# Kernel tuning notes

Measured on AMD Instinct MI355X. Metric: run time of the kernel, lower is better.

Reference implementation:

```python
import jax, jax.numpy as jnp
import numpy as np

EPS = 1e-12  # matches torch euclidean_dist clamp(min=1e-12)


def _euclidean_dist(a, b):
    # pairwise sqrt distances: [N, M]
    d2 = (jnp.sum(a * a, axis=1)[:, None]
          + jnp.sum(b * b, axis=1)[None, :]
          - 2.0 * (a @ b.T))
    return jnp.sqrt(jnp.clip(d2, EPS))


def setup_inputs() -> dict:
    key = jax.random.key(0)
    k1, k2, k3 = jax.random.split(key, 3)
    B, I, E, C = 131072, 512, 128, 64
    x = jax.random.normal(k1, (B, I), dtype=jnp.float32)
    y = jax.random.randint(k2, (B,), 0, C)  # class labels
    W = jax.random.normal(k3, (E, I), dtype=jnp.float32) * 0.02
    b = jnp.zeros((E,), dtype=jnp.float32)
    centroid = jnp.zeros((C, E), dtype=jnp.float32)
    return {"x": x, "y": y, "W": W, "b": b, "centroid": centroid}


def reference(x, y, W, b, centroid):
    # linear projection: [B, E]
    out = x @ W.T + b
    C = centroid.shape[0]
    # fused per-class masked mean (segment mean). flag[i]==0 always in the
    # original module, so the executed update is centroid[i] += mean_i.
    sums = jax.ops.segment_sum(out, y, num_segments=C)            # [C, E]
    counts = jax.ops.segment_sum(jnp.ones(y.shape, out.dtype), y,
                                 num_segments=C)                   # [C]
    means = sums / counts[:, None]
    new_centroid = centroid + means
    # only the final loop iteration's proto_dist / dist survive
    proto_dist = jnp.exp(-0.5 * _euclidean_dist(new_centroid, new_centroid))
    dist = _euclidean_dist(out, new_centroid)                      # [B, C]
    return jax.nn.sigmoid(jnp.exp(-0.5 * dist)), proto_dist
```

## Files before the change

kernel.cpp:

```cpp
#include <hip/hip_runtime.h>
#include <math.h>


typedef __bf16 bf16;
typedef bf16  bf16x4 __attribute__((ext_vector_type(4)));
typedef bf16  bf16x8 __attribute__((ext_vector_type(8)));
typedef float f32x4  __attribute__((ext_vector_type(4)));

#define B_ROWS 131072
#define K_DIM  512
#define E_DIM  128
#define C_CLS  64

#define BM 128
#define BK 64

#define SEG_BLOCKS 256
#define ROWS_PER_SEG (B_ROWS / SEG_BLOCKS)

#define DIST_BLOCKS (B_ROWS / 128)
#define PROTO_BLOCKS 16

__global__ __launch_bounds__(256, 2)
void gemm_kernel(const float* __restrict__ x, const float* __restrict__ W,
                 const float* __restrict__ bias, bf16* __restrict__ outb,
                 float* __restrict__ rnorm)
{
    __shared__ bf16 As[BM * BK];
    __shared__ bf16 Bs[BM * BK];
    __shared__ float lr[BM];

    const int t    = threadIdx.x;
    const int lane = t & 63;
    const int w    = t >> 6;
    const int wr   = w >> 1;
    const int wc   = w & 1;
    const int fr   = lane & 15;
    const int fq   = lane >> 4;
    const long blockRow = (long)blockIdx.x * BM;

    const int srow = t >> 4;
    const int scol = (t & 15) * 4;

    f32x4 acc[4][4] = {};
    if (t < BM) lr[t] = 0.f;

    const float* xg = x + blockRow * K_DIM;

    for (int kt = 0; kt < K_DIM; kt += BK) {
        __syncthreads();
        #pragma unroll
        for (int r = 0; r < 8; ++r) {
            int row = r * 16 + srow;
            f32x4 va = *(const f32x4*)(xg + (long)row * K_DIM + kt + scol);
            f32x4 vb = *(const f32x4*)(W  + (long)row * K_DIM + kt + scol);
            bf16x4 pa = { (bf16)va.x, (bf16)va.y, (bf16)va.z, (bf16)va.w };
            bf16x4 pb = { (bf16)vb.x, (bf16)vb.y, (bf16)vb.z, (bf16)vb.w };
            int byte = row * (BK * 2) + ((scol * 2) ^ ((row & 7) << 4));
            *(bf16x4*)((char*)As + byte) = pa;
            *(bf16x4*)((char*)Bs + byte) = pb;
        }
        __syncthreads();
        #pragma unroll
        for (int kk = 0; kk < 2; ++kk) {
            bf16x8 af[4], bg[4];
            #pragma unroll
            for (int m = 0; m < 4; ++m) {
                int row  = wr * 64 + m * 16 + fr;
                int byte = row * (BK * 2) + (((kk * 32 + fq * 8) * 2) ^ ((row & 7) << 4));
                af[m] = *(const bf16x8*)((const char*)As + byte);
            }
            #pragma unroll
            for (int n = 0; n < 4; ++n) {
                int row  = wc * 64 + n * 16 + fr;
                int byte = row * (BK * 2) + (((kk * 32 + fq * 8) * 2) ^ ((row & 7) << 4));
                bg[n] = *(const bf16x8*)((const char*)Bs + byte);
            }
            #pragma unroll
            for (int m = 0; m < 4; ++m)
                #pragma unroll
                for (int n = 0; n < 4; ++n)
                    acc[m][n] = __builtin_amdgcn_mfma_f32_16x16x32_bf16(
                        af[m], bg[n], acc[m][n], 0, 0, 0);
        }
    }

    float bvv[4];
    #pragma unroll
    for (int n = 0; n < 4; ++n) bvv[n] = bias[wc * 64 + n * 16 + fr];

    #pragma unroll
    for (int m = 0; m < 4; ++m) {
        #pragma unroll
        for (int j = 0; j < 4; ++j) {
            long grow = blockRow + wr * 64 + m * 16 + fq * 4 + j;
            float s = 0.f;
            #pragma unroll
            for (int n = 0; n < 4; ++n) {
                float v = acc[m][n][j] + bvv[n];
                outb[grow * E_DIM + wc * 64 + n * 16 + fr] = (bf16)v;
                s += v * v;
            }
            s += __shfl_xor(s, 1); s += __shfl_xor(s, 2);
            s += __shfl_xor(s, 4); s += __shfl_xor(s, 8);
            if (fr == 0) atomicAdd(&lr[wr * 64 + m * 16 + fq * 4 + j], s);
        }
    }
    __syncthreads();
    if (t < BM) rnorm[blockRow + t] = lr[t];
}

__global__ __launch_bounds__(256)
void segsum_kernel(const bf16* __restrict__ outb, const int* __restrict__ y,
                   float* __restrict__ pw, float* __restrict__ pc)
{
    __shared__ float lsum[C_CLS * E_DIM];
    __shared__ float lcnt[C_CLS];
    const int t = threadIdx.x;
    for (int i = t; i < C_CLS * E_DIM; i += 256) lsum[i] = 0.f;
    if (t < C_CLS) lcnt[t] = 0.f;
    __syncthreads();
    const long base = (long)blockIdx.x * ROWS_PER_SEG;
    const int rsub = t >> 4;
    const int c8   = (t & 15) * 8;
    for (int i = 0; i < ROWS_PER_SEG; i += 16) {
        long row = base + i + rsub;
        int  cls = y[row];
        bf16x8 v = *(const bf16x8*)(outb + row * E_DIM + c8);
        if ((t & 15) == 0) atomicAdd(&lcnt[cls], 1.0f);
        #pragma unroll
        for (int k = 0; k < 8; ++k)
            atomicAdd(&lsum[cls * E_DIM + c8 + k], (float)v[k]);
    }
    __syncthreads();
    for (int i = t; i < C_CLS * E_DIM; i += 256)
        pw[(long)blockIdx.x * (C_CLS * E_DIM) + i] = lsum[i];
    if (t < C_CLS) pc[blockIdx.x * C_CLS + t] = lcnt[t];
}

__global__ __launch_bounds__(256)
void reduce_kernel(const float* __restrict__ pw, float* __restrict__ sums)
{
    int idx = blockIdx.x * 256 + threadIdx.x;
    float s = 0.f;
    for (int j = 0; j < SEG_BLOCKS; ++j) s += pw[(long)j * (C_CLS * E_DIM) + idx];
    sums[idx] = s;
}

__global__ __launch_bounds__(256)
void centroid_kernel(const float* __restrict__ sums, const float* __restrict__ pc,
                     const float* __restrict__ centroid0,
                     float* __restrict__ cent, float* __restrict__ cnorm)
{
    __shared__ float cnt[C_CLS];
    __shared__ float sc[C_CLS * E_DIM];
    const int t = threadIdx.x;
    if (t < C_CLS) {
        float s = 0.f;
        for (int j = 0; j < SEG_BLOCKS; ++j) s += pc[j * C_CLS + t];
        cnt[t] = s;
    }
    __syncthreads();
    for (int i = t; i < C_CLS * E_DIM; i += 256) {
        float v = centroid0[i] + sums[i] / cnt[i >> 7];
        sc[i]   = v;
        cent[i] = v;
    }
    __syncthreads();
    if (t < C_CLS) {
        float s = 0.f;
        for (int e = 0; e < E_DIM; ++e) { float v = sc[t * E_DIM + e]; s += v * v; }
        cnorm[t] = s;
    }
}

__global__ __launch_bounds__(256, 4)
void dist_kernel(const bf16* __restrict__ outb, const float* __restrict__ cent,
                 const float* __restrict__ cnorm, const float* __restrict__ rnorm,
                 float* __restrict__ out0, float* __restrict__ proto)
{
    __shared__ float smemf[C_CLS * 129 + C_CLS + 128];
    const int t = threadIdx.x;

    if (blockIdx.x >= DIST_BLOCKS) {
        float* scf   = smemf;
        float* pnorm = smemf + C_CLS * 129;
        for (int idx = t; idx < C_CLS * E_DIM; idx += 256)
            scf[(idx >> 7) * 129 + (idx & 127)] = cent[idx];
        if (t < C_CLS) pnorm[t] = cnorm[t];
        __syncthreads();
        int p = (blockIdx.x - DIST_BLOCKS) * 256 + t;
        int i = p >> 6, j = p & 63;
        float d = 0.f;
        #pragma unroll 4
        for (int e = 0; e < E_DIM; ++e)
            d += scf[i * 129 + e] * scf[j * 129 + e];
        float d2 = pnorm[i] + pnorm[j] - 2.f * d;
        proto[p] = __expf(-0.5f * sqrtf(fmaxf(d2, 1e-12f)));
        return;
    }

    bf16*  Cs    = (bf16*)smemf;
    float* snorm = smemf + C_CLS * 129;
    float* srnorm = snorm + C_CLS;
    {
        int srw = t >> 5;
        int scl = (t & 31) * 4;
        #pragma unroll
        for (int r = 0; r < 8; ++r) {
            int row = r * 8 + srw;
            f32x4 v = *(const f32x4*)(cent + row * E_DIM + scl);
            bf16x4 pv = { (bf16)v.x, (bf16)v.y, (bf16)v.z, (bf16)v.w };
            int byte = row * (E_DIM * 2) + ((scl * 2) ^ ((row & 7) << 4));
            *(bf16x4*)((char*)Cs + byte) = pv;
        }
        if (t < C_CLS) snorm[t] = cnorm[t];
        if (t < 32) ((f32x4*)srnorm)[t] =
            ((const f32x4*)(rnorm + (long)blockIdx.x * 128))[t];
    }
    const int lane = t & 63;
    const int w    = t >> 6;
    const int fr   = lane & 15;
    const int fq   = lane >> 4;
    const long blkrow = (long)blockIdx.x * 128;
    f32x4 acc[2][4] = {};
    __syncthreads();
    #pragma unroll
    for (int kt = 0; kt < 4; ++kt) {
        bf16x8 af[2];
        #pragma unroll
        for (int m = 0; m < 2; ++m) {
            long row = blkrow + w * 32 + m * 16 + fr;
            af[m] = *(const bf16x8*)(outb + row * E_DIM + kt * 32 + fq * 8);
        }
        #pragma unroll
        for (int n = 0; n < 4; ++n) {
            int row  = n * 16 + fr;
            int byte = row * (E_DIM * 2) + (((kt * 32 + fq * 8) * 2) ^ ((row & 7) << 4));
            bf16x8 bq = *(const bf16x8*)((const char*)Cs + byte);
            acc[0][n] = __builtin_amdgcn_mfma_f32_16x16x32_bf16(af[0], bq, acc[0][n], 0, 0, 0);
            acc[1][n] = __builtin_amdgcn_mfma_f32_16x16x32_bf16(af[1], bq, acc[1][n], 0, 0, 0);
        }
    }
    #pragma unroll
    for (int m = 0; m < 2; ++m) {
        #pragma unroll
        for (int n = 0; n < 4; ++n) {
            int gcol = n * 16 + fr;
            float cn = snorm[gcol];
            #pragma unroll
            for (int j = 0; j < 4; ++j) {
                int lrow = w * 32 + m * 16 + fq * 4 + j;
                float d2 = srnorm[lrow] + cn - 2.f * acc[m][n][j];
                float dist = sqrtf(fmaxf(d2, 1e-12f));
                float ez = __expf(-0.5f * dist);
                out0[(blkrow + lrow) * C_CLS + gcol] = 1.f / (1.f + __expf(-ez));
            }
        }
    }
}

extern "C" void kernel_launch(void* const* d_in, const int* in_sizes, int n_in,
                              void* d_out, int out_size, void* d_ws, size_t ws_size,
                              hipStream_t stream)
{
    const float* x         = (const float*)d_in[0];
    const int*   y         = (const int*)d_in[1];
    const float* W         = (const float*)d_in[2];
    const float* bias      = (const float*)d_in[3];
    const float* centroid0 = (const float*)d_in[4];

    bf16*  outb  = (bf16*)d_ws;
    float* rnorm = (float*)((char*)d_ws + (size_t)B_ROWS * E_DIM * 2);
    float* pw    = rnorm + B_ROWS;
    float* pc    = pw + (long)SEG_BLOCKS * C_CLS * E_DIM;
    float* sums  = pc + SEG_BLOCKS * C_CLS;
    float* cent  = sums + C_CLS * E_DIM;
    float* cnorm = cent + C_CLS * E_DIM;

    float* out0  = (float*)d_out;
    float* proto = out0 + (long)B_ROWS * C_CLS;

    gemm_kernel    <<<B_ROWS / BM, 256, 0, stream>>>(x, W, bias, outb, rnorm);
    segsum_kernel  <<<SEG_BLOCKS, 256, 0, stream>>>(outb, y, pw, pc);
    reduce_kernel  <<<(C_CLS * E_DIM) / 256, 256, 0, stream>>>(pw, sums);
    centroid_kernel<<<1, 256, 0, stream>>>(sums, pc, centroid0, cent, cnorm);
    dist_kernel    <<<DIST_BLOCKS + PROTO_BLOCKS, 256, 0, stream>>>(
        outb, cent, cnorm, rnorm, out0, proto);
}
```

Measured before the change: 192.9 us.

## Double-buffer GEMM tiles, restructure segsum, parallelize reduce and centroid kernels

New measurement: 194.7 us. Within noise of the previous version (+0.9%).

```diff
diff --git a/kernel.cpp b/kernel.cpp
--- a/kernel.cpp
+++ b/kernel.cpp
@@ -3,6 +3,7 @@
 
 
 typedef __bf16 bf16;
+typedef bf16  bf16x2 __attribute__((ext_vector_type(2)));
 typedef bf16  bf16x4 __attribute__((ext_vector_type(4)));
 typedef bf16  bf16x8 __attribute__((ext_vector_type(8)));
 typedef float f32x4  __attribute__((ext_vector_type(4)));
@@ -15,7 +16,7 @@
 #define BM 128
 #define BK 64
 
-#define SEG_BLOCKS 256
+#define SEG_BLOCKS 512
 #define ROWS_PER_SEG (B_ROWS / SEG_BLOCKS)
 
 #define DIST_BLOCKS (B_ROWS / 128)
@@ -26,8 +27,8 @@
                  const float* __restrict__ bias, bf16* __restrict__ outb,
                  float* __restrict__ rnorm)
 {
-    __shared__ bf16 As[BM * BK];
-    __shared__ bf16 Bs[BM * BK];
+    __shared__ bf16 As[2][BM * BK];
+    __shared__ bf16 Bs[2][BM * BK];
     __shared__ float lr[BM];
 
     const int t    = threadIdx.x;
@@ -43,24 +44,41 @@
     const int scol = (t & 15) * 4;
 
     f32x4 acc[4][4] = {};
+    f32x4 va[8], vb[8];
+
+    const float* xg = x + blockRow * K_DIM;
     if (t < BM) lr[t] = 0.f;
 
-    const float* xg = x + blockRow * K_DIM;
-
-    for (int kt = 0; kt < K_DIM; kt += BK) {
-        __syncthreads();
-        #pragma unroll
-        for (int r = 0; r < 8; ++r) {
-            int row = r * 16 + srow;
-            f32x4 va = *(const f32x4*)(xg + (long)row * K_DIM + kt + scol);
-            f32x4 vb = *(const f32x4*)(W  + (long)row * K_DIM + kt + scol);
-            bf16x4 pa = { (bf16)va.x, (bf16)va.y, (bf16)va.z, (bf16)va.w };
-            bf16x4 pb = { (bf16)vb.x, (bf16)vb.y, (bf16)vb.z, (bf16)vb.w };
-            int byte = row * (BK * 2) + ((scol * 2) ^ ((row & 7) << 4));
-            *(bf16x4*)((char*)As + byte) = pa;
-            *(bf16x4*)((char*)Bs + byte) = pb;
-        }
-        __syncthreads();
+    #pragma unroll
+    for (int r = 0; r < 8; ++r) {
+        int row = r * 16 + srow;
+        va[r] = *(const f32x4*)(xg + (long)row * K_DIM + scol);
+        vb[r] = *(const f32x4*)(W  + (long)row * K_DIM + scol);
+    }
+    #pragma unroll
+    for (int r = 0; r < 8; ++r) {
+        int row = r * 16 + srow;
+        bf16x4 pa = { (bf16)va[r].x, (bf16)va[r].y, (bf16)va[r].z, (bf16)va[r].w };
+        bf16x4 pb = { (bf16)vb[r].x, (bf16)vb[r].y, (bf16)vb[r].z, (bf16)vb[r].w };
+        int byte = row * (BK * 2) + ((scol * 2) ^ ((row & 7) << 4));
+        *(bf16x4*)((char*)As[0] + byte) = pa;
+        *(bf16x4*)((char*)Bs[0] + byte) = pb;
+    }
+    __syncthreads();
+
+    for (int kti = 0; kti < K_DIM / BK; ++kti) {
+        const int p = kti & 1;
+        if (kti < K_DIM / BK - 1) {
+            const int kt = (kti + 1) * BK;
+            #pragma unroll
+            for (int r = 0; r < 8; ++r) {
+                int row = r * 16 + srow;
+                va[r] = *(const f32x4*)(xg + (long)row * K_DIM + kt + scol);
+                vb[r] = *(const f32x4*)(W  + (long)row * K_DIM + kt + scol);
+            }
+        }
+        const bf16* Ap = As[p];
+        const bf16* Bp = Bs[p];
         #pragma unroll
         for (int kk = 0; kk < 2; ++kk) {
             bf16x8 af[4], bg[4];
@@ -68,13 +86,13 @@
             for (int m = 0; m < 4; ++m) {
                 int row  = wr * 64 + m * 16 + fr;
                 int byte = row * (BK * 2) + (((kk * 32 + fq * 8) * 2) ^ ((row & 7) << 4));
-                af[m] = *(const bf16x8*)((const char*)As + byte);
+                af[m] = *(const bf16x8*)((const char*)Ap + byte);
             }
             #pragma unroll
             for (int n = 0; n < 4; ++n) {
                 int row  = wc * 64 + n * 16 + fr;
                 int byte = row * (BK * 2) + (((kk * 32 + fq * 8) * 2) ^ ((row & 7) << 4));
-                bg[n] = *(const bf16x8*)((const char*)Bs + byte);
+                bg[n] = *(const bf16x8*)((const char*)Bp + byte);
             }
             #pragma unroll
             for (int m = 0; m < 4; ++m)
@@ -83,6 +101,18 @@
                     acc[m][n] = __builtin_amdgcn_mfma_f32_16x16x32_bf16(
                         af[m], bg[n], acc[m][n], 0, 0, 0);
         }
+        if (kti < K_DIM / BK - 1) {
+            #pragma unroll
+            for (int r = 0; r < 8; ++r) {
+                int row = r * 16 + srow;
+                bf16x4 pa = { (bf16)va[r].x, (bf16)va[r].y, (bf16)va[r].z, (bf16)va[r].w };
+                bf16x4 pb = { (bf16)vb[r].x, (bf16)vb[r].y, (bf16)vb[r].z, (bf16)vb[r].w };
+                int byte = row * (BK * 2) + ((scol * 2) ^ ((row & 7) << 4));
+                *(bf16x4*)((char*)As[p ^ 1] + byte) = pa;
+                *(bf16x4*)((char*)Bs[p ^ 1] + byte) = pb;
+            }
+            __syncthreads();
+        }
     }
 
     float bvv[4];
@@ -116,21 +146,21 @@
 {
     __shared__ float lsum[C_CLS * E_DIM];
     __shared__ float lcnt[C_CLS];
+    __shared__ int   ly[ROWS_PER_SEG];
     const int t = threadIdx.x;
     for (int i = t; i < C_CLS * E_DIM; i += 256) lsum[i] = 0.f;
     if (t < C_CLS) lcnt[t] = 0.f;
-    __syncthreads();
     const long base = (long)blockIdx.x * ROWS_PER_SEG;
-    const int rsub = t >> 4;
-    const int c8   = (t & 15) * 8;
-    for (int i = 0; i < ROWS_PER_SEG; i += 16) {
-        long row = base + i + rsub;
-        int  cls = y[row];
-        bf16x8 v = *(const bf16x8*)(outb + row * E_DIM + c8);
-        if ((t & 15) == 0) atomicAdd(&lcnt[cls], 1.0f);
-        #pragma unroll
-        for (int k = 0; k < 8; ++k)
-            atomicAdd(&lsum[cls * E_DIM + c8 + k], (float)v[k]);
+    if (t < ROWS_PER_SEG) ly[t] = y[base + t];
+    __syncthreads();
+    const int w = t >> 6, lane = t & 63;
+    #pragma unroll 4
+    for (int i = w; i < ROWS_PER_SEG; i += 4) {
+        int cls = ly[i];
+        bf16x2 v = *(const bf16x2*)(outb + (base + i) * E_DIM + lane * 2);
+        atomicAdd(&lsum[cls * E_DIM + lane * 2 + 0], (float)v[0]);
+        atomicAdd(&lsum[cls * E_DIM + lane * 2 + 1], (float)v[1]);
+        if (lane == 0) atomicAdd(&lcnt[cls], 1.f);
     }
     __syncthreads();
     for (int i = t; i < C_CLS * E_DIM; i += 256)
@@ -141,10 +171,22 @@
 __global__ __launch_bounds__(256)
 void reduce_kernel(const float* __restrict__ pw, float* __restrict__ sums)
 {
-    int idx = blockIdx.x * 256 + threadIdx.x;
+    __shared__ float red[256];
+    const int t = threadIdx.x;
+    const int idx = blockIdx.x * 32 + (t & 31);
+    const int js  = t >> 5;
     float s = 0.f;
-    for (int j = 0; j < SEG_BLOCKS; ++j) s += pw[(long)j * (C_CLS * E_DIM) + idx];
-    sums[idx] = s;
+    #pragma unroll 8
+    for (int j = js * 64; j < js * 64 + 64; ++j)
+        s += pw[(long)j * (C_CLS * E_DIM) + idx];
+    red[t] = s;
+    __syncthreads();
+    if (t < 32) {
+        float r = red[t];
+        #pragma unroll
+        for (int k = 1; k < 8; ++k) r += red[t + 32 * k];
+        sums[blockIdx.x * 32 + t] = r;
+    }
 }
 
 __global__ __launch_bounds__(256)
@@ -152,26 +194,32 @@
                      const float* __restrict__ centroid0,
                      float* __restrict__ cent, float* __restrict__ cnorm)
 {
-    __shared__ float cnt[C_CLS];
-    __shared__ float sc[C_CLS * E_DIM];
+    __shared__ float red[256];
+    const int c = blockIdx.x;
     const int t = threadIdx.x;
-    if (t < C_CLS) {
-        float s = 0.f;
-        for (int j = 0; j < SEG_BLOCKS; ++j) s += pc[j * C_CLS + t];
-        cnt[t] = s;
-    }
-    __syncthreads();
-    for (int i = t; i < C_CLS * E_DIM; i += 256) {
-        float v = centroid0[i] + sums[i] / cnt[i >> 7];
-        sc[i]   = v;
-        cent[i] = v;
-    }
-    __syncthreads();
-    if (t < C_CLS) {
-        float s = 0.f;
-        for (int e = 0; e < E_DIM; ++e) { float v = sc[t * E_DIM + e]; s += v * v; }
-        cnorm[t] = s;
-    }
+    float s = pc[t * C_CLS + c] + pc[(t + 256) * C_CLS + c];
+    red[t] = s;
+    __syncthreads();
+    #pragma unroll
+    for (int st = 128; st > 0; st >>= 1) {
+        if (t < st) red[t] += red[t + st];
+        __syncthreads();
+    }
+    const float cnt = red[0];
+    __syncthreads();
+    float v = 0.f;
+    if (t < E_DIM) {
+        v = centroid0[c * E_DIM + t] + sums[c * E_DIM + t] / cnt;
+        cent[c * E_DIM + t] = v;
+    }
+    red[t] = v * v;
+    __syncthreads();
+    #pragma unroll
+    for (int st = 64; st > 0; st >>= 1) {
+        if (t < st) red[t] += red[t + st];
+        __syncthreads();
+    }
+    if (t == 0) cnorm[c] = red[0];
 }
 
 __global__ __launch_bounds__(256, 4)
@@ -200,8 +248,8 @@
         return;
     }
 
-    bf16*  Cs    = (bf16*)smemf;
-    float* snorm = smemf + C_CLS * 129;
+    bf16*  Cs     = (bf16*)smemf;
+    float* snorm  = smemf + C_CLS * 129;
     float* srnorm = snorm + C_CLS;
     {
         int srw = t >> 5;
@@ -283,8 +331,8 @@
 
     gemm_kernel    <<<B_ROWS / BM, 256, 0, stream>>>(x, W, bias, outb, rnorm);
     segsum_kernel  <<<SEG_BLOCKS, 256, 0, stream>>>(outb, y, pw, pc);
-    reduce_kernel  <<<(C_CLS * E_DIM) / 256, 256, 0, stream>>>(pw, sums);
-    centroid_kernel<<<1, 256, 0, stream>>>(sums, pc, centroid0, cent, cnorm);
+    reduce_kernel  <<<(C_CLS * E_DIM) / 32, 256, 0, stream>>>(pw, sums);
+    centroid_kernel<<<C_CLS, 256, 0, stream>>>(sums, pc, centroid0, cent, cnorm);
     dist_kernel    <<<DIST_BLOCKS + PROTO_BLOCKS, 256, 0, stream>>>(
         outb, cent, cnorm, rnorm, out0, proto);
 }
```
